# Optimization experiments

Measured on AMD Instinct MI355X. Metric: run time of the kernel, lower is better.

Reference implementation:

```python
import jax, jax.numpy as jnp
import numpy as np

N_NODES = 100000
N_EDGES = 1600000


def gcn_conv(x, edge_index, W, b):
    # PyG GCNConv: add self-loops, symmetric degree normalization,
    # linear transform, scatter-sum aggregation, + bias.
    n = x.shape[0]
    loop = jnp.arange(n, dtype=edge_index.dtype)
    src = jnp.concatenate([edge_index[0], loop])
    dst = jnp.concatenate([edge_index[1], loop])
    deg = jnp.zeros((n,), x.dtype).at[dst].add(1.0)
    dinv = jnp.where(deg > 0, deg ** -0.5, 0.0)
    norm = dinv[src] * dinv[dst]            # [E+N]
    h = x @ W                               # [N, out]
    msg = h[src] * norm[:, None]            # gather + scale
    out = jax.ops.segment_sum(msg, dst, num_segments=n)
    return out + b


def setup_inputs() -> dict:
    key = jax.random.key(0)
    k1, k2, k3, k4 = jax.random.split(key, 4)
    d_in, d_lat, d_out = 512, 128, 64
    x = jax.random.normal(k1, (N_NODES, d_in), jnp.float32)
    edge_index = jax.random.randint(k2, (2, N_EDGES), 0, N_NODES, jnp.int64)
    W1 = jax.random.normal(k3, (d_in, d_lat), jnp.float32) * (d_in ** -0.5)
    b1 = jnp.zeros((d_lat,), jnp.float32)
    W2 = jax.random.normal(k4, (d_lat, d_out), jnp.float32) * (d_lat ** -0.5)
    b2 = jnp.zeros((d_out,), jnp.float32)
    return {"x": x, "edge_index": edge_index, "W1": W1, "b1": b1, "W2": W2, "b2": b2}


def reference(x, edge_index, W1, b1, W2, b2):
    h = gcn_conv(x, edge_index, W1, b1)
    h = gcn_conv(h, edge_index, W2, b2)
    return jax.nn.relu(h)
```

## Files before the change

kernel.cpp:

```cpp
#include <hip/hip_runtime.h>
#include <hip/hip_bf16.h>

typedef unsigned short u16;
typedef unsigned int   u32;

#define N_NODES 100000
#define N_EDGES 1600000
#define NQ      (N_EDGES / 4)
#define SLICE   12500
#define BPG     96

__device__ __forceinline__ float bf2f(u16 u) {
    union { u32 i; float f; } c; c.i = ((u32)u) << 16; return c.f;
}
__device__ __forceinline__ u16 f2bf(float f) {
    union { float f; u32 i; } c; c.f = f;
    u32 u = c.i;
    u += 0x7fffu + ((u >> 16) & 1u);
    return (u16)(u >> 16);
}
__device__ __forceinline__ void acc8(uint4 d, float* a) {
    a[0] += bf2f((u16)(d.x & 0xffffu)); a[1] += bf2f((u16)(d.x >> 16));
    a[2] += bf2f((u16)(d.y & 0xffffu)); a[3] += bf2f((u16)(d.y >> 16));
    a[4] += bf2f((u16)(d.z & 0xffffu)); a[5] += bf2f((u16)(d.z >> 16));
    a[6] += bf2f((u16)(d.w & 0xffffu)); a[7] += bf2f((u16)(d.w >> 16));
}

__global__ void k_detect(const u32* __restrict__ ei, int* __restrict__ flag) {
    if (threadIdx.x == 0 && blockIdx.x == 0) {
        u32 h = ei[1] | ei[3] | ei[5] | ei[7];
        *flag = (h == 0u) ? 1 : 0;
    }
}

__global__ __launch_bounds__(256) void k_convert(const u32* __restrict__ ei,
                                                 const int* __restrict__ flag,
                                                 uint4* __restrict__ src4,
                                                 uint4* __restrict__ dst4) {
    int q = blockIdx.x * 256 + threadIdx.x;
    if (q >= NQ) return;
    const uint4* e4 = (const uint4*)ei;
    if (*flag) {
        uint4 a = e4[2 * q],          b = e4[2 * q + 1];
        src4[q] = make_uint4(a.x, a.z, b.x, b.z);
        uint4 c = e4[2 * NQ + 2 * q], d = e4[2 * NQ + 2 * q + 1];
        dst4[q] = make_uint4(c.x, c.z, d.x, d.z);
    } else {
        src4[q] = e4[q];
        dst4[q] = e4[NQ + q];
    }
}

__global__ __launch_bounds__(256) void k_degree(const uint4* __restrict__ dst4,
                                                int* __restrict__ deg) {
    const int g = blockIdx.x & 7, bb = blockIdx.x >> 3;
    const int lo = g * SLICE, hi = lo + SLICE;
    for (int q = bb * 256 + threadIdx.x; q < NQ; q += BPG * 256) {
        uint4 d = dst4[q];
        if ((int)d.x >= lo && (int)d.x < hi) atomicAdd(&deg[d.x], 1);
        if ((int)d.y >= lo && (int)d.y < hi) atomicAdd(&deg[d.y], 1);
        if ((int)d.z >= lo && (int)d.z < hi) atomicAdd(&deg[d.z], 1);
        if ((int)d.w >= lo && (int)d.w < hi) atomicAdd(&deg[d.w], 1);
    }
}

__global__ void k_scan_part(const int* __restrict__ deg, int* __restrict__ rowstart,
                            int* __restrict__ bsums) {
    __shared__ int sh[256];
    const int t = threadIdx.x, b = blockIdx.x;
    const int base = b * 2048 + t * 8;
    int v[8]; int s = 0;
#pragma unroll
    for (int i = 0; i < 8; i++) {
        int idx = base + i;
        v[i] = (idx < N_NODES) ? deg[idx] : 0;
        s += v[i];
    }
    sh[t] = s;
    __syncthreads();
    for (int d = 1; d < 256; d <<= 1) {
        int x = (t >= d) ? sh[t - d] : 0;
        __syncthreads();
        sh[t] += x;
        __syncthreads();
    }
    int acc = sh[t] - s;
#pragma unroll
    for (int i = 0; i < 8; i++) {
        int idx = base + i;
        if (idx < N_NODES) rowstart[idx] = acc;
        acc += v[i];
    }
    if (t == 255) bsums[b] = sh[255];
}

__global__ void k_scan_sums(const int* __restrict__ bsums, int* __restrict__ boffs, int nb) {
    if (threadIdx.x == 0 && blockIdx.x == 0) {
        int r = 0;
        for (int i = 0; i < nb; i++) { boffs[i] = r; r += bsums[i]; }
    }
}

__global__ void k_scan_add_dinv(int* __restrict__ rowstart, const int* __restrict__ boffs,
                                const int* __restrict__ deg, float* __restrict__ dinv,
                                int* __restrict__ cursor) {
    int i = blockIdx.x * blockDim.x + threadIdx.x;
    if (i < N_NODES) {
        int r = rowstart[i] + boffs[i >> 11];
        rowstart[i] = r;
        cursor[i] = r;
        dinv[i] = rsqrtf((float)(deg[i] + 1));
    }
    if (i == 0) rowstart[N_NODES] = N_EDGES;
}

__global__ __launch_bounds__(256) void k_fill(const uint4* __restrict__ dst4,
                                              const int* __restrict__ src32,
                                              int* __restrict__ cursor,
                                              int* __restrict__ csr) {
    const int g = blockIdx.x & 7, bb = blockIdx.x >> 3;
    const int lo = g * SLICE, hi = lo + SLICE;
    for (int q = bb * 256 + threadIdx.x; q < NQ; q += BPG * 256) {
        uint4 d = dst4[q];
        if ((int)d.x >= lo && (int)d.x < hi) csr[atomicAdd(&cursor[d.x], 1)] = src32[4 * q];
        if ((int)d.y >= lo && (int)d.y < hi) csr[atomicAdd(&cursor[d.y], 1)] = src32[4 * q + 1];
        if ((int)d.z >= lo && (int)d.z < hi) csr[atomicAdd(&cursor[d.z], 1)] = src32[4 * q + 2];
        if ((int)d.w >= lo && (int)d.w < hi) csr[atomicAdd(&cursor[d.w], 1)] = src32[4 * q + 3];
    }
}


__global__ void k_w12(const float* __restrict__ W1, const float* __restrict__ W2,
                      float* __restrict__ W12f) {
    int idx = blockIdx.x * 256 + threadIdx.x;
    int k = idx >> 6, n = idx & 63;
    float acc = 0.f;
#pragma unroll 4
    for (int j = 0; j < 128; j++) acc += W1[k * 128 + j] * W2[j * 64 + n];
    W12f[idx] = acc;
}

__global__ void k_c1(const float* __restrict__ b1, const float* __restrict__ W2,
                     float* __restrict__ c1) {
    int n = threadIdx.x;
    float acc = 0.f;
    for (int j = 0; j < 128; j++) acc += b1[j] * W2[j * 64 + n];
    c1[n] = acc;
}

__global__ void k_fragB(const float* __restrict__ W12f, u16* __restrict__ Bt) {
    int idx = blockIdx.x * 256 + threadIdx.x;
    int l = idx & 63, c = (idx >> 6) & 3, kt = idx >> 8;
    int n = c * 16 + (l & 15);
    int k0 = kt * 32 + (l >> 4) * 8;
    u32 p[4];
#pragma unroll
    for (int j = 0; j < 4; j++) {
        u16 a = f2bf(W12f[(k0 + 2 * j) * 64 + n]);
        u16 b = f2bf(W12f[(k0 + 2 * j + 1) * 64 + n]);
        p[j] = (u32)a | ((u32)b << 16);
    }
    *(uint4*)&Bt[(long)idx * 8] = make_uint4(p[0], p[1], p[2], p[3]);
}


__global__ __launch_bounds__(256) void gemm_x(const float* __restrict__ A,
                                              const u16* __restrict__ Bt,
                                              const float* __restrict__ dinv,
                                              u16* __restrict__ C, int M) {
    constexpr int SA = 40;
    __shared__ u16 As[128 * SA];
    typedef __attribute__((ext_vector_type(8))) short v8s;
    typedef __attribute__((ext_vector_type(4))) float v4f;

    const int t = threadIdx.x;
    const int wave = t >> 6, lane = t & 63;
    const int m = lane & 15, quad = lane >> 4;
    const int row0 = blockIdx.x * 128;

    v4f acc[2][4];
#pragma unroll
    for (int i = 0; i < 2; i++)
#pragma unroll
        for (int c = 0; c < 4; c++)
#pragma unroll
            for (int r = 0; r < 4; r++) acc[i][c][r] = 0.0f;

    const int arow = t >> 1, ahalf = t & 1;
    const long aoff = (long)(row0 + arow) * 512;
    const bool arow_ok = (row0 + arow) < M;

    for (int kt = 0; kt < 16; ++kt) {
        const int kk0 = kt * 32 + ahalf * 16;
        float4 f0 = make_float4(0.f, 0.f, 0.f, 0.f), f1 = f0, f2 = f0, f3 = f0;
        if (arow_ok) {
            f0 = *(const float4*)&A[aoff + kk0];
            f1 = *(const float4*)&A[aoff + kk0 + 4];
            f2 = *(const float4*)&A[aoff + kk0 + 8];
            f3 = *(const float4*)&A[aoff + kk0 + 12];
        }
        uint4 w0, w1;
        w0.x = (u32)f2bf(f0.x) | ((u32)f2bf(f0.y) << 16);
        w0.y = (u32)f2bf(f0.z) | ((u32)f2bf(f0.w) << 16);
        w0.z = (u32)f2bf(f1.x) | ((u32)f2bf(f1.y) << 16);
        w0.w = (u32)f2bf(f1.z) | ((u32)f2bf(f1.w) << 16);
        w1.x = (u32)f2bf(f2.x) | ((u32)f2bf(f2.y) << 16);
        w1.y = (u32)f2bf(f2.z) | ((u32)f2bf(f2.w) << 16);
        w1.z = (u32)f2bf(f3.x) | ((u32)f2bf(f3.y) << 16);
        w1.w = (u32)f2bf(f3.z) | ((u32)f2bf(f3.w) << 16);
        *(uint4*)&As[arow * SA + ahalf * 16] = w0;
        *(uint4*)&As[arow * SA + ahalf * 16 + 8] = w1;
        __syncthreads();
        v8s a0 = *(const v8s*)&As[(wave * 32 + m) * SA + quad * 8];
        v8s a1 = *(const v8s*)&As[(wave * 32 + 16 + m) * SA + quad * 8];
#pragma unroll
        for (int c = 0; c < 4; c++) {
            v8s b = *(const v8s*)&Bt[(long)((kt * 4 + c) * 64 + lane) * 8];
            acc[0][c] = __builtin_amdgcn_mfma_f32_16x16x32_bf16(a0, b, acc[0][c], 0, 0, 0);
            acc[1][c] = __builtin_amdgcn_mfma_f32_16x16x32_bf16(a1, b, acc[1][c], 0, 0, 0);
        }
        __syncthreads();
    }
#pragma unroll
    for (int i = 0; i < 2; i++)
#pragma unroll
        for (int r = 0; r < 4; r++) {
            int grow = row0 + wave * 32 + i * 16 + quad * 4 + r;
            if (grow < M) {
                float w = dinv[grow];
#pragma unroll
                for (int c = 0; c < 4; c++)
                    C[(long)grow * 64 + c * 16 + m] = f2bf(acc[i][c][r] * w);
            }
        }
}


__global__ __launch_bounds__(256) void agg_a(const u16* __restrict__ zp,
                                             const float* __restrict__ dinv,
                                             const int* __restrict__ rowstart,
                                             const int* __restrict__ csr,
                                             u16* __restrict__ yp,
                                             float* __restrict__ sfac) {
    const int wave = threadIdx.x >> 6, lane = threadIdx.x & 63;
    const int n = blockIdx.x * 4 + wave;
    const int g = lane >> 3, l = lane & 7;
    const uint4* z4 = (const uint4*)zp;
    float a[8] = {0.f, 0.f, 0.f, 0.f, 0.f, 0.f, 0.f, 0.f};
    float sd = 0.f;
    const float w0 = dinv[n];
    if (g == 0) {
        acc8(z4[(long)n * 8 + l], a);
        sd = w0;
    }
    const int i1 = rowstart[n + 1];
    int i = rowstart[n] + g;
    for (; i + 8 < i1; i += 16) {
        int s0 = csr[i], s1 = csr[i + 8];
        uint4 d0 = z4[(long)s0 * 8 + l];
        uint4 d1 = z4[(long)s1 * 8 + l];
        sd += dinv[s0] + dinv[s1];
        acc8(d0, a); acc8(d1, a);
    }
    for (; i < i1; i += 8) {
        int s = csr[i];
        uint4 d = z4[(long)s * 8 + l];
        sd += dinv[s];
        acc8(d, a);
    }
#pragma unroll
    for (int j = 0; j < 8; j++) {
        a[j] += __shfl_xor(a[j], 8);
        a[j] += __shfl_xor(a[j], 16);
        a[j] += __shfl_xor(a[j], 32);
    }
    sd += __shfl_xor(sd, 8); sd += __shfl_xor(sd, 16); sd += __shfl_xor(sd, 32);
    if (g == 0) {
        float w2 = w0 * w0;
        uint4 o;
        o.x = (u32)f2bf(a[0] * w2) | ((u32)f2bf(a[1] * w2) << 16);
        o.y = (u32)f2bf(a[2] * w2) | ((u32)f2bf(a[3] * w2) << 16);
        o.z = (u32)f2bf(a[4] * w2) | ((u32)f2bf(a[5] * w2) << 16);
        o.w = (u32)f2bf(a[6] * w2) | ((u32)f2bf(a[7] * w2) << 16);
        ((uint4*)yp)[(long)n * 8 + l] = o;
        if (l == 0) sfac[n] = w0 * sd;
    }
}


__global__ __launch_bounds__(256) void agg_b(const u16* __restrict__ yp,
                                             const float* __restrict__ dinv,
                                             const int* __restrict__ rowstart,
                                             const int* __restrict__ csr,
                                             const float* __restrict__ sfac,
                                             const float* __restrict__ c1,
                                             const float* __restrict__ b2,
                                             float* __restrict__ out) {
    const int wave = threadIdx.x >> 6, lane = threadIdx.x & 63;
    const int n = blockIdx.x * 4 + wave;
    const int g = lane >> 3, l = lane & 7;
    const uint4* y4 = (const uint4*)yp;
    float a[8] = {0.f, 0.f, 0.f, 0.f, 0.f, 0.f, 0.f, 0.f};
    if (g == 0) acc8(y4[(long)n * 8 + l], a);
    const int i1 = rowstart[n + 1];
    int i = rowstart[n] + g;
    for (; i + 8 < i1; i += 16) {
        int s0 = csr[i], s1 = csr[i + 8];
        uint4 d0 = y4[(long)s0 * 8 + l];
        uint4 d1 = y4[(long)s1 * 8 + l];
        acc8(d0, a); acc8(d1, a);
    }
    for (; i < i1; i += 8) {
        uint4 d = y4[(long)csr[i] * 8 + l];
        acc8(d, a);
    }
#pragma unroll
    for (int j = 0; j < 8; j++) {
        a[j] += __shfl_xor(a[j], 8);
        a[j] += __shfl_xor(a[j], 16);
        a[j] += __shfl_xor(a[j], 32);
    }
    if (g == 0) {
        const float w0 = dinv[n];
        const float sn = sfac[n];
        float4 c0 = ((const float4*)c1)[2 * l], c4 = ((const float4*)c1)[2 * l + 1];
        float4 b0 = ((const float4*)b2)[2 * l], b4 = ((const float4*)b2)[2 * l + 1];
        float4 r0, r1;
        r0.x = fmaxf(a[0] * w0 + sn * c0.x + b0.x, 0.f);
        r0.y = fmaxf(a[1] * w0 + sn * c0.y + b0.y, 0.f);
        r0.z = fmaxf(a[2] * w0 + sn * c0.z + b0.z, 0.f);
        r0.w = fmaxf(a[3] * w0 + sn * c0.w + b0.w, 0.f);
        r1.x = fmaxf(a[4] * w0 + sn * c4.x + b4.x, 0.f);
        r1.y = fmaxf(a[5] * w0 + sn * c4.y + b4.y, 0.f);
        r1.z = fmaxf(a[6] * w0 + sn * c4.z + b4.z, 0.f);
        r1.w = fmaxf(a[7] * w0 + sn * c4.w + b4.w, 0.f);
        ((float4*)out)[(long)n * 16 + 2 * l]     = r0;
        ((float4*)out)[(long)n * 16 + 2 * l + 1] = r1;
    }
}


extern "C" void kernel_launch(void* const* d_in, const int* in_sizes, int n_in,
                              void* d_out, int out_size, void* d_ws, size_t ws_size,
                              hipStream_t stream) {
    const float* x  = (const float*)d_in[0];
    const u32*   ei = (const u32*)d_in[1];
    const float* W1 = (const float*)d_in[2];
    const float* b1 = (const float*)d_in[3];
    const float* W2 = (const float*)d_in[4];
    const float* b2 = (const float*)d_in[5];
    float* out = (float*)d_out;

    char* ws = (char*)d_ws;
    size_t o = 0;
    auto alloc = [&](size_t bytes) -> char* {
        char* p = ws + o;
        o = (o + bytes + 255) & ~(size_t)255;
        return p;
    };
    int*   deg      = (int*)  alloc(N_NODES * 4);
    float* dinv     = (float*)alloc(N_NODES * 4);
    int*   rowstart = (int*)  alloc((N_NODES + 1) * 4);
    int*   cursor   = (int*)  alloc(N_NODES * 4);
    int*   bsums    = (int*)  alloc(64 * 4);
    int*   boffs    = (int*)  alloc(64 * 4);
    int*   eflag    = (int*)  alloc(256);
    float* W12f     = (float*)alloc(512 * 64 * 4);
    u16*   Bt       = (u16*)  alloc(512 * 64 * 2);
    float* c1       = (float*)alloc(64 * 4);
    float* sfac     = (float*)alloc(N_NODES * 4);
    uint4* src4     = (uint4*)alloc((size_t)N_EDGES * 4);
    uint4* dst4     = (uint4*)alloc((size_t)N_EDGES * 4);
    int*   csr      = (int*)  alloc((size_t)N_EDGES * 4);
    u16*   z        = (u16*)  alloc((size_t)N_NODES * 64 * 2);
    u16*   y        = (u16*)  alloc((size_t)N_NODES * 64 * 2);
    (void)ws_size;

    hipMemsetAsync(deg, 0, N_NODES * 4, stream);

    const int NB = (N_NODES + 255) / 256;
    const int CQ = (NQ + 255) / 256;
    const int SCAN_BLKS = (N_NODES + 2047) / 2048;

    k_detect<<<1, 64, 0, stream>>>(ei, eflag);
    k_convert<<<CQ, 256, 0, stream>>>(ei, eflag, src4, dst4);
    k_degree<<<8 * BPG, 256, 0, stream>>>(dst4, deg);
    k_scan_part<<<SCAN_BLKS, 256, 0, stream>>>(deg, rowstart, bsums);
    k_scan_sums<<<1, 64, 0, stream>>>(bsums, boffs, SCAN_BLKS);
    k_scan_add_dinv<<<NB, 256, 0, stream>>>(rowstart, boffs, deg, dinv, cursor);
    k_fill<<<8 * BPG, 256, 0, stream>>>(dst4, (const int*)src4, cursor, csr);

    k_w12<<<128, 256, 0, stream>>>(W1, W2, W12f);
    k_c1<<<1, 64, 0, stream>>>(b1, W2, c1);
    k_fragB<<<16, 256, 0, stream>>>(W12f, Bt);

    gemm_x<<<(N_NODES + 127) / 128, 256, 0, stream>>>(x, Bt, dinv, z, N_NODES);
    agg_a<<<N_NODES / 4, 256, 0, stream>>>(z, dinv, rowstart, csr, y, sfac);
    agg_b<<<N_NODES / 4, 256, 0, stream>>>(y, dinv, rowstart, csr, sfac, c1, b2, out);
}
```

Measured before the change: 572.5 us.

## Slice feature dimension into 4 column blocks for cache-friendly gather aggregation

The GEMM output is now stored feature-sliced: four slices of 16 bf16 columns, each slice contiguous across nodes. The aggregation kernels then process one slice per block group, with 16 lanes per node instead of 64. This shrinks the gathered working set per pass to about 3.2 MB per slice, so random neighbor gathers can hit in L2/MALL. The cost is that CSR indices are re-read four times and there are more blocks. The block-offset scan is also switched from a serial single-thread loop to a wave shuffle scan.

```diff
diff --git a/kernel.cpp b/kernel.cpp
--- a/kernel.cpp
+++ b/kernel.cpp
@@ -9,6 +9,10 @@
 #define NQ      (N_EDGES / 4)
 #define SLICE   12500
 #define BPG     96
+
+#define FSLICES 4
+#define NPB     16
+#define BLKS_PER_SLICE (N_NODES / NPB)
 
 __device__ __forceinline__ float bf2f(u16 u) {
     union { u32 i; float f; } c; c.i = ((u32)u) << 16; return c.f;
@@ -95,10 +99,14 @@
 }
 
 __global__ void k_scan_sums(const int* __restrict__ bsums, int* __restrict__ boffs, int nb) {
-    if (threadIdx.x == 0 && blockIdx.x == 0) {
-        int r = 0;
-        for (int i = 0; i < nb; i++) { boffs[i] = r; r += bsums[i]; }
-    }
+    int l = threadIdx.x;
+    int v = (l < nb) ? bsums[l] : 0;
+    int x = v;
+    for (int d = 1; d < 64; d <<= 1) {
+        int u = __shfl_up(x, d);
+        if (l >= d) x += u;
+    }
+    if (l < nb) boffs[l] = x - v;
 }
 
 __global__ void k_scan_add_dinv(int* __restrict__ rowstart, const int* __restrict__ boffs,
@@ -230,7 +238,7 @@
                 float w = dinv[grow];
 #pragma unroll
                 for (int c = 0; c < 4; c++)
-                    C[(long)grow * 64 + c * 16 + m] = f2bf(acc[i][c][r] * w);
+                    C[((long)c * M + grow) * 16 + m] = f2bf(acc[i][c][r] * w);
             }
         }
 }
@@ -242,39 +250,59 @@
                                              const int* __restrict__ csr,
                                              u16* __restrict__ yp,
                                              float* __restrict__ sfac) {
+    const int s  = blockIdx.x / BLKS_PER_SLICE;
+    const int nb = blockIdx.x % BLKS_PER_SLICE;
     const int wave = threadIdx.x >> 6, lane = threadIdx.x & 63;
-    const int n = blockIdx.x * 4 + wave;
-    const int g = lane >> 3, l = lane & 7;
-    const uint4* z4 = (const uint4*)zp;
+    const int sub = lane >> 4;
+    const int sl  = lane & 15;
+    const int g   = sl >> 1, h = sl & 1;
+    const int n   = nb * NPB + wave * 4 + sub;
+    const uint4* z4 = (const uint4*)zp + (long)s * N_NODES * 2;
+
     float a[8] = {0.f, 0.f, 0.f, 0.f, 0.f, 0.f, 0.f, 0.f};
     float sd = 0.f;
     const float w0 = dinv[n];
     if (g == 0) {
-        acc8(z4[(long)n * 8 + l], a);
-        sd = w0;
+        acc8(z4[(long)n * 2 + h], a);
+        if (s == 0 && h == 0) sd = w0;
     }
     const int i1 = rowstart[n + 1];
     int i = rowstart[n] + g;
-    for (; i + 8 < i1; i += 16) {
-        int s0 = csr[i], s1 = csr[i + 8];
-        uint4 d0 = z4[(long)s0 * 8 + l];
-        uint4 d1 = z4[(long)s1 * 8 + l];
-        sd += dinv[s0] + dinv[s1];
-        acc8(d0, a); acc8(d1, a);
-    }
-    for (; i < i1; i += 8) {
-        int s = csr[i];
-        uint4 d = z4[(long)s * 8 + l];
-        sd += dinv[s];
-        acc8(d, a);
+    if (s == 0) {
+        for (; i + 8 < i1; i += 16) {
+            int s0 = csr[i], s1 = csr[i + 8];
+            uint4 d0 = z4[(long)s0 * 2 + h];
+            uint4 d1 = z4[(long)s1 * 2 + h];
+            if (h == 0) sd += dinv[s0] + dinv[s1];
+            acc8(d0, a); acc8(d1, a);
+        }
+        for (; i < i1; i += 8) {
+            int s0 = csr[i];
+            uint4 d = z4[(long)s0 * 2 + h];
+            if (h == 0) sd += dinv[s0];
+            acc8(d, a);
+        }
+    } else {
+        for (; i + 8 < i1; i += 16) {
+            int s0 = csr[i], s1 = csr[i + 8];
+            uint4 d0 = z4[(long)s0 * 2 + h];
+            uint4 d1 = z4[(long)s1 * 2 + h];
+            acc8(d0, a); acc8(d1, a);
+        }
+        for (; i < i1; i += 8) {
+            uint4 d = z4[(long)csr[i] * 2 + h];
+            acc8(d, a);
+        }
     }
 #pragma unroll
     for (int j = 0; j < 8; j++) {
+        a[j] += __shfl_xor(a[j], 2);
+        a[j] += __shfl_xor(a[j], 4);
         a[j] += __shfl_xor(a[j], 8);
-        a[j] += __shfl_xor(a[j], 16);
-        a[j] += __shfl_xor(a[j], 32);
-    }
-    sd += __shfl_xor(sd, 8); sd += __shfl_xor(sd, 16); sd += __shfl_xor(sd, 32);
+    }
+    if (s == 0) {
+        sd += __shfl_xor(sd, 2); sd += __shfl_xor(sd, 4); sd += __shfl_xor(sd, 8);
+    }
     if (g == 0) {
         float w2 = w0 * w0;
         uint4 o;
@@ -282,8 +310,8 @@
         o.y = (u32)f2bf(a[2] * w2) | ((u32)f2bf(a[3] * w2) << 16);
         o.z = (u32)f2bf(a[4] * w2) | ((u32)f2bf(a[5] * w2) << 16);
         o.w = (u32)f2bf(a[6] * w2) | ((u32)f2bf(a[7] * w2) << 16);
-        ((uint4*)yp)[(long)n * 8 + l] = o;
-        if (l == 0) sfac[n] = w0 * sd;
+        ((uint4*)yp)[(long)s * N_NODES * 2 + (long)n * 2 + h] = o;
+        if (s == 0 && h == 0) sfac[n] = w0 * sd;
     }
 }
 
@@ -296,35 +324,42 @@
                                              const float* __restrict__ c1,
                                              const float* __restrict__ b2,
                                              float* __restrict__ out) {
+    const int s  = blockIdx.x / BLKS_PER_SLICE;
+    const int nb = blockIdx.x % BLKS_PER_SLICE;
     const int wave = threadIdx.x >> 6, lane = threadIdx.x & 63;
-    const int n = blockIdx.x * 4 + wave;
-    const int g = lane >> 3, l = lane & 7;
-    const uint4* y4 = (const uint4*)yp;
+    const int sub = lane >> 4;
+    const int sl  = lane & 15;
+    const int g   = sl >> 1, h = sl & 1;
+    const int n   = nb * NPB + wave * 4 + sub;
+    const uint4* y4 = (const uint4*)yp + (long)s * N_NODES * 2;
+
     float a[8] = {0.f, 0.f, 0.f, 0.f, 0.f, 0.f, 0.f, 0.f};
-    if (g == 0) acc8(y4[(long)n * 8 + l], a);
+    if (g == 0) acc8(y4[(long)n * 2 + h], a);
     const int i1 = rowstart[n + 1];
     int i = rowstart[n] + g;
     for (; i + 8 < i1; i += 16) {
         int s0 = csr[i], s1 = csr[i + 8];
-        uint4 d0 = y4[(long)s0 * 8 + l];
-        uint4 d1 = y4[(long)s1 * 8 + l];
+        uint4 d0 = y4[(long)s0 * 2 + h];
+        uint4 d1 = y4[(long)s1 * 2 + h];
         acc8(d0, a); acc8(d1, a);
     }
     for (; i < i1; i += 8) {
-        uint4 d = y4[(long)csr[i] * 8 + l];
+        uint4 d = y4[(long)csr[i] * 2 + h];
         acc8(d, a);
     }
 #pragma unroll
     for (int j = 0; j < 8; j++) {
+        a[j] += __shfl_xor(a[j], 2);
+        a[j] += __shfl_xor(a[j], 4);
         a[j] += __shfl_xor(a[j], 8);
-        a[j] += __shfl_xor(a[j], 16);
-        a[j] += __shfl_xor(a[j], 32);
     }
     if (g == 0) {
         const float w0 = dinv[n];
         const float sn = sfac[n];
-        float4 c0 = ((const float4*)c1)[2 * l], c4 = ((const float4*)c1)[2 * l + 1];
-        float4 b0 = ((const float4*)b2)[2 * l], b4 = ((const float4*)b2)[2 * l + 1];
+        float4 c0 = ((const float4*)c1)[s * 4 + h * 2];
+        float4 c4 = ((const float4*)c1)[s * 4 + h * 2 + 1];
+        float4 b0 = ((const float4*)b2)[s * 4 + h * 2];
+        float4 b4 = ((const float4*)b2)[s * 4 + h * 2 + 1];
         float4 r0, r1;
         r0.x = fmaxf(a[0] * w0 + sn * c0.x + b0.x, 0.f);
         r0.y = fmaxf(a[1] * w0 + sn * c0.y + b0.y, 0.f);
@@ -334,8 +369,8 @@
         r1.y = fmaxf(a[5] * w0 + sn * c4.y + b4.y, 0.f);
         r1.z = fmaxf(a[6] * w0 + sn * c4.z + b4.z, 0.f);
         r1.w = fmaxf(a[7] * w0 + sn * c4.w + b4.w, 0.f);
-        ((float4*)out)[(long)n * 16 + 2 * l]     = r0;
-        ((float4*)out)[(long)n * 16 + 2 * l + 1] = r1;
+        ((float4*)out)[(long)n * 16 + s * 4 + h * 2]     = r0;
+        ((float4*)out)[(long)n * 16 + s * 4 + h * 2 + 1] = r1;
     }
 }
 
@@ -395,6 +430,6 @@
     k_fragB<<<16, 256, 0, stream>>>(W12f, Bt);
 
     gemm_x<<<(N_NODES + 127) / 128, 256, 0, stream>>>(x, Bt, dinv, z, N_NODES);
-    agg_a<<<N_NODES / 4, 256, 0, stream>>>(z, dinv, rowstart, csr, y, sfac);
-    agg_b<<<N_NODES / 4, 256, 0, stream>>>(y, dinv, rowstart, csr, sfac, c1, b2, out);
-}
+    agg_a<<<FSLICES * BLKS_PER_SLICE, 256, 0, stream>>>(z, dinv, rowstart, csr, y, sfac);
+    agg_b<<<FSLICES * BLKS_PER_SLICE, 256, 0, stream>>>(y, dinv, rowstart, csr, sfac, c1, b2, out);
+}
```

After: 593.7 us. 3.7% more time.
